# Kernel tuning notes

Hardware: AMD Instinct MI355X
Metric: run time of the kernel (lower is better)

## Reference

```python
import jax, jax.numpy as jnp
import numpy as np

B, S, NH, HID, NL = 64, 512, 16, 512, 16
W_WIN, PAD, THR, BW = 5, 2, 5.0, 0.1
D_IN = 1 + 2 * NH


def setup_inputs():
    key = jax.random.key(0)
    ks = jax.random.split(key, 16)
    time = jax.random.uniform(ks[0], (B, S)) * 1000.0
    mag = 15.0 + jax.random.normal(ks[1], (B, S))
    err = 0.01 + 0.1 * jax.random.uniform(ks[2], (B, S))
    sc = 0.05
    p = {}
    p["light_curve"] = jnp.stack([time, mag, err], axis=1)  # (B,3,S)
    p["valid_mask"] = jnp.ones((B, S), dtype=bool)
    p["frequency"] = 0.5 + 4.5 * jax.random.uniform(ks[3], (B,))
    p["W_ih0"] = sc * jax.random.normal(ks[4], (3 * HID, D_IN))
    p["b_ih0"] = jnp.zeros((3 * HID,))
    p["W_hh0"] = sc * jax.random.normal(ks[5], (3 * HID, HID))
    p["b_hh0"] = jnp.zeros((3 * HID,))
    p["W_ih1"] = sc * jax.random.normal(ks[6], (3 * HID, HID))
    p["b_ih1"] = jnp.zeros((3 * HID,))
    p["W_hh1"] = sc * jax.random.normal(ks[7], (3 * HID, HID))
    p["b_hh1"] = jnp.zeros((3 * HID,))
    p["Wl1"] = sc * jax.random.normal(ks[8], (HID, HID))
    p["bl1"] = jnp.zeros((HID,))
    p["Wl2"] = sc * jax.random.normal(ks[9], (NL, HID))
    p["bl2"] = jnp.zeros((NL,))
    return p


def _flag_outliers(phase, mag):
    # Sorted-window weighted (Epanechnikov in circular phase-delta) mean/std outlier test.
    # Caller guarantees all points valid (setup uses an all-True mask), so index_select == identity.
    perm = jnp.argsort(phase)
    ps, ms = phase[perm], mag[perm]

    def windows(x):
        xp = jnp.concatenate([x[-PAD:], x, x[:PAD]])  # circular pad
        return jnp.stack([xp[i:i + S] for i in range(W_WIN)], axis=-1)  # (S, w)

    wp, wm = windows(ps), windows(ms)
    cols = jnp.array([i for i in range(W_WIN) if i != PAD])
    dphi = wp[:, cols] - wp[:, PAD:PAD + 1]
    dphi = jnp.remainder(dphi - 0.5, 1.0) - 0.5
    wgt = 0.75 * (1.0 - dphi ** 2)
    wmm = wm[:, cols]
    wsum = wgt.sum(-1)
    loc = (wmm * wgt).sum(-1) / wsum
    scale = jnp.sqrt((((wmm - loc[:, None]) ** 2) * wgt).sum(-1) / (wsum - 1.0))
    thr = loc + THR * scale
    sigma = jnp.zeros_like(mag).at[perm].set(thr)  # inverse-permute (index_copy_)
    return mag > sigma


def _gru_layer(x, W_ih, b_ih, W_hh, b_hh):
    # torch nn.GRU cell math; x: (B,S,D) -> (B,S,H)
    xW = jnp.einsum('bsd,gd->bsg', x, W_ih) + b_ih  # (B,S,3H)

    def step(h, xt):
        hW = h @ W_hh.T + b_hh
        xr, xz, xn = jnp.split(xt, 3, axis=-1)
        hr, hz, hn = jnp.split(hW, 3, axis=-1)
        r = jax.nn.sigmoid(xr + hr)
        z = jax.nn.sigmoid(xz + hz)
        n = jnp.tanh(xn + r * hn)
        h = (1.0 - z) * n + z * h
        return h, h

    h0 = jnp.zeros((x.shape[0], W_hh.shape[1]), x.dtype)
    _, hs = jax.lax.scan(step, h0, jnp.swapaxes(xW, 0, 1))
    return jnp.swapaxes(hs, 0, 1)


def reference(light_curve, valid_mask, frequency, W_ih0, b_ih0, W_hh0, b_hh0,
              W_ih1, b_ih1, W_hh1, b_hh1, Wl1, bl1, Wl2, bl2):
    time, mag, err = light_curve[:, 0], light_curve[:, 1], light_curve[:, 2]
    period = 2.0 / frequency[:, None]  # fold_with_double_period=True (default)
    phase = jnp.remainder(time, period) / period
    outlier = jax.vmap(_flag_outliers)(phase, mag)
    is_valid = valid_mask & ~outlier

    # periodic-kernel interpolation on 50-point grid; align phase to brightness max
    grid = jnp.linspace(0.0, 1.0, 50)
    delta = grid[None, :, None] - phase[:, None, :]  # (B,50,S)
    K = jnp.exp((jnp.cos(2.0 * jnp.pi * delta) - 1.0) / BW ** 2)
    Wk = is_valid[:, None, :].astype(K.dtype) * K
    Wk = Wk / Wk.sum(-1, keepdims=True)
    smooth = (Wk * mag[:, None, :]).sum(-1)  # (B,50)
    phase = phase - grid[jnp.argmax(smooth, axis=-1)][:, None]

    # sort by phase, invalid points last; scaler=None -> loc 0, scale 1
    big = jnp.finfo(jnp.float32).max
    idx = jnp.argsort(jnp.where(is_valid, phase, big), axis=-1)
    phase = jnp.take_along_axis(phase, idx, -1)
    mag = jnp.take_along_axis(mag, idx, -1)
    is_valid = jnp.take_along_axis(is_valid, idx, -1)

    # Fourier phase embedding [cos_1..cos_H, sin_1..sin_H] + mag -> (B,S,2H+1)
    k = jnp.arange(1, NH + 1, dtype=phase.dtype)
    ang = 2.0 * jnp.pi * phase[:, :, None] * k
    emb = jnp.concatenate([jnp.cos(ang), jnp.sin(ang), mag[:, :, None]], axis=-1)

    ht = _gru_layer(emb, W_ih0, b_ih0, W_hh0, b_hh0)
    ht = _gru_layer(ht, W_ih1, b_ih1, W_hh1, b_hh1)

    m = is_valid[:, :, None].astype(ht.dtype)  # context='average'
    ctx = (ht * m).sum(1) / m.sum(1)
    h1 = jax.nn.gelu(ctx @ Wl1.T + bl1, approximate=False)
    z = h1 @ Wl2.T + bl2
    return z
```

## Files before the change

### kernel.cpp

```cpp
#include <hip/hip_runtime.h>


typedef unsigned short u16;
typedef unsigned int u32;
typedef unsigned long long u64;

__device__ __forceinline__ float b2f(u16 u) { return __uint_as_float(((u32)u) << 16); }
__device__ __forceinline__ float blo(u32 u) { return __uint_as_float(u << 16); }
__device__ __forceinline__ float bhi(u32 u) { return __uint_as_float(u & 0xffff0000u); }
__device__ __forceinline__ u16 f2b(float f) {
    u32 x = __float_as_uint(f);
    u32 r = x + 0x7fffu + ((x >> 16) & 1u);
    return (u16)(r >> 16);
}

#define SS 512
#define TWO_PI 6.28318530717958647692f
#define BIGF 3.402823466e+38f
#define PANEL_ELEMS (1536 * 512)
#define FLAGS_BYTES 32768
#define FL(g, f) (((g) * 16 + (f)) * 16)
#define F_A 0
#define F_B 2
#define F_C 4
#define G_A 6
#define G_B 8
#define G_C 10
#define F_PRE 12
#define F_CTX 14

struct P {
    const void* lc;
    const void* freq;
    const void* W[12];
    void* out;
    void* ws;
    unsigned long long ws_size;
};

__device__ __forceinline__ bool inputs_are_bf16(const void* freq) {
    const u16* q = (const u16*)freq;
    bool ok = true;
    for (int i = 0; i < 64; ++i) {
        float v = b2f(q[i]);
        ok = ok && (v >= 0.4f) && (v <= 5.5f);
    }
    return ok;
}

template<bool BF>
__device__ __forceinline__ float ldw(const void* p, size_t i) {
    if constexpr (BF) return b2f(((const u16*)p)[i]);
    else              return ((const float*)p)[i];
}
template<bool BF>
__device__ __forceinline__ const void* rowp(const void* base, int row) {
    if constexpr (BF) return (const void*)((const u16*)base + (size_t)row * 512);
    else              return (const void*)((const float*)base + (size_t)row * 512);
}

__device__ __forceinline__ void sc_store_f(float* ptr, float v) {
    __hip_atomic_store(ptr, v, __ATOMIC_RELAXED, __HIP_MEMORY_SCOPE_AGENT);
}
__device__ __forceinline__ float sc_load_f(const float* ptr) {
    return __hip_atomic_load(ptr, __ATOMIC_RELAXED, __HIP_MEMORY_SCOPE_AGENT);
}
__device__ __forceinline__ void sc_store_i(int* ptr, int v) {
    __hip_atomic_store(ptr, v, __ATOMIC_RELAXED, __HIP_MEMORY_SCOPE_AGENT);
}
__device__ __forceinline__ int sc_load_i(const int* ptr) {
    return __hip_atomic_load(ptr, __ATOMIC_RELAXED, __HIP_MEMORY_SCOPE_AGENT);
}
__device__ __forceinline__ void waitge(const int* f, int v, int* dead) {
    if (*dead) return;
    int it = 0;
    while (sc_load_i(f) < v) {
        __builtin_amdgcn_s_sleep(1);
        if (++it > 400000) { *dead = 1; break; }
    }
}

template<bool BF>
__device__ void build_panel_one(const void* W, int tid, char* panbase) {
    if constexpr (BF) {
        const uint4* Ws = (const uint4*)W;
        uint4* panel = (uint4*)panbase;
        for (int i = tid; i < 1536 * 64; i += 512) {
            int r = i >> 6, k8 = i & 63;
            panel[(size_t)k8 * 1536 + r] = Ws[i];
        }
    } else {
        const float4* Ws = (const float4*)W;
        float4* panel = (float4*)panbase;
        for (int i = tid; i < 1536 * 128; i += 512) {
            int r = i >> 7, k4 = i & 127;
            panel[(size_t)k4 * 1536 + r] = Ws[i];
        }
    }
}
template<bool BF>
__device__ void build_piece(const void* W, int half, int tid, char* panbase) {
    if constexpr (BF) {
        const uint4* Ws = (const uint4*)W;
        uint4* panel = (uint4*)panbase;
        for (int i = tid; i < 768 * 64; i += 512) {
            int r768 = i >> 6, k8 = i & 63;
            int g3 = r768 >> 8, r = r768 & 255;
            int srcrow = g3 * 512 + half * 256 + r;
            panel[(size_t)k8 * 768 + r768] = Ws[(size_t)srcrow * 64 + k8];
        }
    } else {
        const float4* Ws = (const float4*)W;
        float4* panel = (float4*)panbase;
        for (int i = tid; i < 768 * 128; i += 512) {
            int r768 = i >> 7, k4 = i & 127;
            int g3 = r768 >> 8, r = r768 & 255;
            int srcrow = g3 * 512 + half * 256 + r;
            panel[(size_t)k4 * 768 + r768] = Ws[(size_t)srcrow * 128 + k4];
        }
    }
}

template<bool BF>
__device__ __forceinline__ void tridot_panel(const void* panel, int j,
                                             const float* __restrict__ sh,
                                             float& ar, float& az, float& an) {
    if constexpr (BF) {
        const uint4* pr = (const uint4*)panel + j;
        const uint4* pz = pr + 512;
        const uint4* pn = pr + 1024;
        for (int k0 = 0; k0 < 512; k0 += 8) {
            size_t o = (size_t)(k0 >> 3) * 1536;
            float4 h0 = *(const float4*)&sh[k0];
            float4 h1 = *(const float4*)&sh[k0 + 4];
            uint4 a = pr[o], c = pz[o], d = pn[o];
            ar += blo(a.x) * h0.x + bhi(a.x) * h0.y + blo(a.y) * h0.z + bhi(a.y) * h0.w
                + blo(a.z) * h1.x + bhi(a.z) * h1.y + blo(a.w) * h1.z + bhi(a.w) * h1.w;
            az += blo(c.x) * h0.x + bhi(c.x) * h0.y + blo(c.y) * h0.z + bhi(c.y) * h0.w
                + blo(c.z) * h1.x + bhi(c.z) * h1.y + blo(c.w) * h1.z + bhi(c.w) * h1.w;
            an += blo(d.x) * h0.x + bhi(d.x) * h0.y + blo(d.y) * h0.z + bhi(d.y) * h0.w
                + blo(d.z) * h1.x + bhi(d.z) * h1.y + blo(d.w) * h1.z + bhi(d.w) * h1.w;
        }
    } else {
        const float4* pr = (const float4*)panel + j;
        const float4* pz = pr + 512;
        const float4* pn = pr + 1024;
        for (int k0 = 0; k0 < 512; k0 += 8) {
            size_t o = (size_t)(k0 >> 2) * 1536;
            float4 h0 = *(const float4*)&sh[k0];
            float4 h1 = *(const float4*)&sh[k0 + 4];
            float4 a0 = pr[o], a1 = pr[o + 1536];
            float4 c0 = pz[o], c1 = pz[o + 1536];
            float4 d0 = pn[o], d1 = pn[o + 1536];
            ar += a0.x * h0.x + a0.y * h0.y + a0.z * h0.z + a0.w * h0.w
                + a1.x * h1.x + a1.y * h1.y + a1.z * h1.z + a1.w * h1.w;
            az += c0.x * h0.x + c0.y * h0.y + c0.z * h0.z + c0.w * h0.w
                + c1.x * h1.x + c1.y * h1.y + c1.z * h1.z + c1.w * h1.w;
            an += d0.x * h0.x + d0.y * h0.y + d0.z * h0.z + d0.w * h0.w
                + d1.x * h1.x + d1.y * h1.y + d1.z * h1.z + d1.w * h1.w;
        }
    }
}

template<bool BF>
__device__ __forceinline__ void tridot2(const void* panel, int r, int kh,
                                        const float* __restrict__ ha,
                                        const float* __restrict__ hb,
                                        float& a0r, float& a0z, float& a0n,
                                        float& a1r, float& a1z, float& a1n) {
    const int kbeg = kh * 256;
    if constexpr (BF) {
        const uint4* pr = (const uint4*)panel + r;
        const uint4* pz = pr + 256;
        const uint4* pn = pr + 512;
        for (int k0 = kbeg; k0 < kbeg + 256; k0 += 8) {
            size_t o = (size_t)(k0 >> 3) * 768;
            float4 ha0 = *(const float4*)&ha[k0];
            float4 ha1 = *(const float4*)&ha[k0 + 4];
            float4 hb0 = *(const float4*)&hb[k0];
            float4 hb1 = *(const float4*)&hb[k0 + 4];
            uint4 a = pr[o], c = pz[o], d = pn[o];
            a0r += blo(a.x)*ha0.x + bhi(a.x)*ha0.y + blo(a.y)*ha0.z + bhi(a.y)*ha0.w
                 + blo(a.z)*ha1.x + bhi(a.z)*ha1.y + blo(a.w)*ha1.z + bhi(a.w)*ha1.w;
            a1r += blo(a.x)*hb0.x + bhi(a.x)*hb0.y + blo(a.y)*hb0.z + bhi(a.y)*hb0.w
                 + blo(a.z)*hb1.x + bhi(a.z)*hb1.y + blo(a.w)*hb1.z + bhi(a.w)*hb1.w;
            a0z += blo(c.x)*ha0.x + bhi(c.x)*ha0.y + blo(c.y)*ha0.z + bhi(c.y)*ha0.w
                 + blo(c.z)*ha1.x + bhi(c.z)*ha1.y + blo(c.w)*ha1.z + bhi(c.w)*ha1.w;
            a1z += blo(c.x)*hb0.x + bhi(c.x)*hb0.y + blo(c.y)*hb0.z + bhi(c.y)*hb0.w
                 + blo(c.z)*hb1.x + bhi(c.z)*hb1.y + blo(c.w)*hb1.z + bhi(c.w)*hb1.w;
            a0n += blo(d.x)*ha0.x + bhi(d.x)*ha0.y + blo(d.y)*ha0.z + bhi(d.y)*ha0.w
                 + blo(d.z)*ha1.x + bhi(d.z)*ha1.y + blo(d.w)*ha1.z + bhi(d.w)*ha1.w;
            a1n += blo(d.x)*hb0.x + bhi(d.x)*hb0.y + blo(d.y)*hb0.z + bhi(d.y)*hb0.w
                 + blo(d.z)*hb1.x + bhi(d.z)*hb1.y + blo(d.w)*hb1.z + bhi(d.w)*hb1.w;
        }
    } else {
        const float4* pr = (const float4*)panel + r;
        const float4* pz = pr + 256;
        const float4* pn = pr + 512;
        for (int k0 = kbeg; k0 < kbeg + 256; k0 += 8) {
            size_t o = (size_t)(k0 >> 2) * 768;
            float4 ha0 = *(const float4*)&ha[k0];
            float4 ha1 = *(const float4*)&ha[k0 + 4];
            float4 hb0 = *(const float4*)&hb[k0];
            float4 hb1 = *(const float4*)&hb[k0 + 4];
            float4 a0 = pr[o], a1 = pr[o + 768];
            float4 c0 = pz[o], c1 = pz[o + 768];
            float4 d0 = pn[o], d1 = pn[o + 768];
            a0r += a0.x*ha0.x + a0.y*ha0.y + a0.z*ha0.z + a0.w*ha0.w
                 + a1.x*ha1.x + a1.y*ha1.y + a1.z*ha1.z + a1.w*ha1.w;
            a1r += a0.x*hb0.x + a0.y*hb0.y + a0.z*hb0.z + a0.w*hb0.w
                 + a1.x*hb1.x + a1.y*hb1.y + a1.z*hb1.z + a1.w*hb1.w;
            a0z += c0.x*ha0.x + c0.y*ha0.y + c0.z*ha0.z + c0.w*ha0.w
                 + c1.x*ha1.x + c1.y*ha1.y + c1.z*ha1.z + c1.w*ha1.w;
            a1z += c0.x*hb0.x + c0.y*hb0.y + c0.z*hb0.z + c0.w*hb0.w
                 + c1.x*hb1.x + c1.y*hb1.y + c1.z*hb1.z + c1.w*hb1.w;
            a0n += d0.x*ha0.x + d0.y*ha0.y + d0.z*ha0.z + d0.w*ha0.w
                 + d1.x*ha1.x + d1.y*ha1.y + d1.z*ha1.z + d1.w*ha1.w;
            a1n += d0.x*hb0.x + d0.y*hb0.y + d0.z*hb0.z + d0.w*hb0.w
                 + d1.x*hb1.x + d1.y*hb1.y + d1.z*hb1.z + d1.w*hb1.w;
        }
    }
}

template<bool BF>
__device__ __forceinline__ float dot512(const void* vr, const float* __restrict__ sh) {
    float acc = 0.f;
    if constexpr (BF) {
        const u32* pr = (const u32*)vr;
        for (int k0 = 0; k0 < 512; k0 += 8) {
            float4 h0 = *(const float4*)&sh[k0];
            float4 h1 = *(const float4*)&sh[k0 + 4];
            uint4 a = *(const uint4*)(pr + (k0 >> 1));
            acc += blo(a.x) * h0.x + bhi(a.x) * h0.y + blo(a.y) * h0.z + bhi(a.y) * h0.w
                 + blo(a.z) * h1.x + bhi(a.z) * h1.y + blo(a.w) * h1.z + bhi(a.w) * h1.w;
        }
    } else {
        const float* pr = (const float*)vr;
        for (int k0 = 0; k0 < 512; k0 += 8) {
            float4 h0 = *(const float4*)&sh[k0];
            float4 h1 = *(const float4*)&sh[k0 + 4];
            float4 a0 = *(const float4*)(pr + k0), a1 = *(const float4*)(pr + k0 + 4);
            acc += a0.x * h0.x + a0.y * h0.y + a0.z * h0.z + a0.w * h0.w
                 + a1.x * h1.x + a1.y * h1.y + a1.z * h1.z + a1.w * h1.w;
        }
    }
    return acc;
}

struct PreShm {
    float ph[512], mg[512], skey[512], sig[512], vld[512];
    int   sidx[512];
    float ps2[512], ms2[512], vs2[512];
    float pn[50][8], pd[50][8], smoothv[50];
    float gshift, nv;
};

__device__ void bitonic512(float* skey, int* sidx, int tid) {
    for (int k = 2; k <= 512; k <<= 1) {
        for (int j = k >> 1; j > 0; j >>= 1) {
            int ixj = tid ^ j;
            if (ixj > tid) {
                float ka = skey[tid], kb = skey[ixj];
                int ia = sidx[tid], ib = sidx[ixj];
                bool up = ((tid & k) == 0);
                bool agtb = (ka > kb) || (ka == kb && ia > ib);
                if (agtb == up) {
                    skey[tid] = kb; skey[ixj] = ka;
                    sidx[tid] = ib; sidx[ixj] = ia;
                }
            }
            __syncthreads();
        }
    }
}

template<bool BF>
__device__ void preproc_core(const P& p, PreShm& s, int b, int tid) {
    float period = 2.0f / ldw<BF>(p.freq, b);
    float t = ldw<BF>(p.lc, (size_t)b * 3 * SS + tid);
    float m = ldw<BF>(p.lc, (size_t)b * 3 * SS + SS + tid);
    float ph0 = fmodf(t, period) / period;
    s.ph[tid] = ph0; s.mg[tid] = m;
    s.skey[tid] = ph0; s.sidx[tid] = tid;
    __syncthreads();
    bitonic512(s.skey, s.sidx, tid);
    {
        float pc = s.skey[tid];
        float wv[4], mv[4];
        float wsum = 0.f, wm = 0.f;
        const int offs[4] = {-2, -1, 1, 2};
#pragma unroll
        for (int c = 0; c < 4; ++c) {
            int jj = (tid + offs[c]) & 511;
            float d = s.skey[jj] - pc;
            float u = d - 0.5f; u = u - floorf(u);
            float dphi = u - 0.5f;
            float w = 0.75f * (1.0f - dphi * dphi);
            float mm = s.mg[s.sidx[jj]];
            wv[c] = w; mv[c] = mm;
            wsum += w; wm += w * mm;
        }
        float loc = wm / wsum;
        float s2 = 0.f;
#pragma unroll
        for (int c = 0; c < 4; ++c) { float dm = mv[c] - loc; s2 += dm * dm * wv[c]; }
        float scale = sqrtf(s2 / (wsum - 1.0f));
        s.sig[s.sidx[tid]] = loc + 5.0f * scale;
    }
    __syncthreads();
    s.vld[tid] = (s.mg[tid] > s.sig[tid]) ? 0.0f : 1.0f;
    __syncthreads();
    if (tid == 0) {
        float acc = 0.f;
        for (int i = 0; i < 512; ++i) acc += s.vld[i];
        s.nv = acc;
    }
    {
        int g = tid >> 3, pq = tid & 7;
        if (g < 50) {
            float gv = (float)g * (1.0f / 49.0f);
            float num = 0.f, den = 0.f;
            int s0 = pq * 64;
            for (int ss = s0; ss < s0 + 64; ++ss) {
                float d = gv - s.ph[ss];
                float c = cosf(TWO_PI * d);
                float K = expf((c - 1.0f) * 100.0f);
                float w = s.vld[ss] * K;
                den += w; num += w * s.mg[ss];
            }
            s.pn[g][pq] = num; s.pd[g][pq] = den;
        }
    }
    __syncthreads();
    if (tid < 50) {
        float num = 0.f, den = 0.f;
#pragma unroll
        for (int c = 0; c < 8; ++c) { num += s.pn[tid][c]; den += s.pd[tid][c]; }
        s.smoothv[tid] = num / den;
    }
    __syncthreads();
    if (tid == 0) {
        float best = s.smoothv[0]; int bi = 0;
        for (int g = 1; g < 50; ++g) if (s.smoothv[g] > best) { best = s.smoothv[g]; bi = g; }
        s.gshift = (float)bi * (1.0f / 49.0f);
    }
    __syncthreads();
    float p2 = s.ph[tid] - s.gshift;
    s.ph[tid] = p2;
    s.skey[tid] = (s.vld[tid] > 0.f) ? p2 : BIGF;
    s.sidx[tid] = tid;
    __syncthreads();
    bitonic512(s.skey, s.sidx, tid);
    {
        int o = s.sidx[tid];
        s.ps2[tid] = s.ph[o]; s.ms2[tid] = s.mg[o]; s.vs2[tid] = s.vld[o];
    }
    __syncthreads();
}

struct ShmA {
    PreShm pre;
    float psb[2][512], msb[2][512];
    float h0L[1024];
    float eL[2][34];
    float part[6][256];
    float xp[3][256];
};
struct ShmB { float h0loc[1024]; float part[6][256]; };
struct ShmC {
    float h1L[1024]; float vs2L[2][512]; float nvL[2];
    float ctxL[512], gL[512]; float part[6][256];
};
struct ShmOldA { PreShm pre; float h0[512], h1[512], eL[34]; };
struct ShmU {
    union { ShmA a; ShmB b; ShmC c; ShmOldA o; } u;
    int dead;
};

template<bool BF, bool PAN>
__device__ void run_all(const P& p, ShmU& S) {
    PreShm& pre = S.u.o.pre;
    float* h0 = S.u.o.h0;
    float* h1 = S.u.o.h1;
    float* eL = S.u.o.eL;
    int b = blockIdx.x, tid = threadIdx.x;
    char* panbase = (char*)p.ws + FLAGS_BYTES;
    const size_t PMAT = (size_t)PANEL_ELEMS * (BF ? 2 : 4);

    if constexpr (PAN) {
        build_panel_one<BF>(p.W[2], tid, panbase);
        build_panel_one<BF>(p.W[4], tid, panbase + PMAT);
        build_panel_one<BF>(p.W[6], tid, panbase + 2 * PMAT);
        __threadfence();
    }
    preproc_core<BF>(p, pre, b, tid);

    int j = tid;
    float wr0[33], wz0[33], wn0[33];
#pragma unroll
    for (int d = 0; d < 33; ++d) {
        wr0[d] = ldw<BF>(p.W[0], (size_t)j * 33 + d);
        wz0[d] = ldw<BF>(p.W[0], ((size_t)j + 512) * 33 + d);
        wn0[d] = ldw<BF>(p.W[0], ((size_t)j + 1024) * 33 + d);
    }
    float bi0r = ldw<BF>(p.W[1], j), bi0z = ldw<BF>(p.W[1], j + 512), bi0n = ldw<BF>(p.W[1], j + 1024);
    float bh0r = ldw<BF>(p.W[3], j), bh0z = ldw<BF>(p.W[3], j + 512), bh0n = ldw<BF>(p.W[3], j + 1024);
    float bi1r = ldw<BF>(p.W[5], j), bi1z = ldw<BF>(p.W[5], j + 512), bi1n = ldw<BF>(p.W[5], j + 1024);
    float bh1r = ldw<BF>(p.W[7], j), bh1z = ldw<BF>(p.W[7], j + 512), bh1n = ldw<BF>(p.W[7], j + 1024);

    const void* pan0  = (const void*)panbase;
    const void* pan1x = (const void*)(panbase + PMAT);
    const void* pan1h = (const void*)(panbase + 2 * PMAT);
    const void *w0r = rowp<BF>(p.W[2], j), *w0z = rowp<BF>(p.W[2], j + 512), *w0n = rowp<BF>(p.W[2], j + 1024);
    const void *x1r = rowp<BF>(p.W[4], j), *x1z = rowp<BF>(p.W[4], j + 512), *x1n = rowp<BF>(p.W[4], j + 1024);
    const void *w1r = rowp<BF>(p.W[6], j), *w1z = rowp<BF>(p.W[6], j + 512), *w1n = rowp<BF>(p.W[6], j + 1024);

    h0[j] = 0.f; h1[j] = 0.f;
    float cacc = 0.f;
    __syncthreads();

    for (int tt = 0; tt < 512; ++tt) {
        if (j < 16) {
            float ang = TWO_PI * pre.ps2[tt] * (float)(j + 1);
            float sv, cv; sincosf(ang, &sv, &cv);
            eL[j] = cv; eL[16 + j] = sv;
        }
        if (j == 32) eL[32] = pre.ms2[tt];
        __syncthreads();
        float xr = bi0r, xz = bi0z, xn = bi0n;
#pragma unroll
        for (int d = 0; d < 33; ++d) {
            float e = eL[d];
            xr += wr0[d] * e; xz += wz0[d] * e; xn += wn0[d] * e;
        }
        float ar = bh0r, az = bh0z, an = bh0n;
        if constexpr (PAN) tridot_panel<BF>(pan0, j, h0, ar, az, an);
        else {
            for (int k = 0; k < 512; ++k) {
                float h = h0[k];
                ar += ldw<BF>(w0r, k) * h; az += ldw<BF>(w0z, k) * h; an += ldw<BF>(w0n, k) * h;
            }
        }
        float h0prev = h0[j];
        float r0 = 1.0f / (1.0f + expf(-(xr + ar)));
        float z0 = 1.0f / (1.0f + expf(-(xz + az)));
        float n0 = tanhf(xn + r0 * an);
        float nh0 = (1.0f - z0) * n0 + z0 * h0prev;
        __syncthreads();
        h0[j] = nh0;
        __syncthreads();
        float yr = bi1r, yz = bi1z, yn = bi1n;
        float cr = bh1r, cz = bh1z, cn = bh1n;
        if constexpr (PAN) {
            tridot_panel<BF>(pan1x, j, h0, yr, yz, yn);
            tridot_panel<BF>(pan1h, j, h1, cr, cz, cn);
        } else {
            for (int k = 0; k < 512; ++k) {
                float h = h0[k], g = h1[k];
                yr += ldw<BF>(x1r, k) * h; yz += ldw<BF>(x1z, k) * h; yn += ldw<BF>(x1n, k) * h;
                cr += ldw<BF>(w1r, k) * g; cz += ldw<BF>(w1z, k) * g; cn += ldw<BF>(w1n, k) * g;
            }
        }
        float h1prev = h1[j];
        float r1 = 1.0f / (1.0f + expf(-(yr + cr)));
        float z1 = 1.0f / (1.0f + expf(-(yz + cz)));
        float n1 = tanhf(yn + r1 * cn);
        float nh1 = (1.0f - z1) * n1 + z1 * h1prev;
        cacc += pre.vs2[tt] * nh1;
        __syncthreads();
        h1[j] = nh1;
    }
    __syncthreads();

    h0[j] = cacc / pre.nv;
    __syncthreads();
    float a1 = ldw<BF>(p.W[9], j) + dot512<BF>(rowp<BF>(p.W[8], j), h0);
    float g = 0.5f * a1 * (1.0f + erff(a1 * 0.70710678118654752440f));
    __syncthreads();
    h1[j] = g;
    __syncthreads();
    if (j < 16) {
        float a2 = ldw<BF>(p.W[11], j) + dot512<BF>(rowp<BF>(p.W[10], j), h1);
        if constexpr (BF) ((u16*)p.out)[(size_t)b * 16 + j] = f2b(a2);
        else              ((float*)p.out)[(size_t)b * 16 + j] = a2;
    }
}

__global__ __launch_bounds__(512) void fused_kernel_old(P p) {
    __shared__ ShmU S;
    bool bf = inputs_are_bf16(p.freq);
    u64 PMAT = bf ? 1572864ull : 3145728ull;
    bool pan = (p.ws && p.ws_size >= (u64)FLAGS_BYTES + 3 * PMAT);
    if (bf) { if (pan) run_all<true, true>(p, S);  else run_all<true, false>(p, S); }
    else    { if (pan) run_all<false, true>(p, S); else run_all<false, false>(p, S); }
}


template<bool BF>
__device__ void runA(const P& p, ShmU& S, int g, int hf, int tid, char* pan,
                     float* h0r, float* pp, int* flags) {
    int* dead = &S.dead;
    build_piece<BF>(p.W[2], hf, tid, pan);
    __threadfence();
    int myb = 2 * g + hf, ob = 2 * g + (1 - hf);
    preproc_core<BF>(p, S.u.a.pre, myb, tid);
    sc_store_f(&pp[(size_t)myb * 2048 + tid], S.u.a.pre.ps2[tid]);
    sc_store_f(&pp[(size_t)myb * 2048 + 512 + tid], S.u.a.pre.ms2[tid]);
    sc_store_f(&pp[(size_t)myb * 2048 + 1024 + tid], S.u.a.pre.vs2[tid]);
    if (tid == 0) sc_store_f(&pp[(size_t)myb * 2048 + 1536], S.u.a.pre.nv);
    asm volatile("s_waitcnt vmcnt(0)" ::: "memory");
    __syncthreads();
    if (tid == 0) sc_store_i(&flags[FL(g, F_PRE + hf)], 1);
    S.u.a.psb[hf][tid] = S.u.a.pre.ps2[tid];
    S.u.a.msb[hf][tid] = S.u.a.pre.ms2[tid];
    if (tid == 0) waitge(&flags[FL(g, F_PRE + (1 - hf))], 1, dead);
    __syncthreads();
    S.u.a.psb[1 - hf][tid] = sc_load_f(&pp[(size_t)ob * 2048 + tid]);
    S.u.a.msb[1 - hf][tid] = sc_load_f(&pp[(size_t)ob * 2048 + 512 + tid]);

    const int r = tid & 255, kh = tid >> 8;
    const int j = hf * 256 + r;
    const float bi0r = ldw<BF>(p.W[1], j), bi0z = ldw<BF>(p.W[1], j + 512), bi0n = ldw<BF>(p.W[1], j + 1024);
    const float bh0r = ldw<BF>(p.W[3], j), bh0z = ldw<BF>(p.W[3], j + 512), bh0n = ldw<BF>(p.W[3], j + 1024);

    float* h0L = S.u.a.h0L;
    h0L[tid] = 0.f; h0L[tid + 512] = 0.f;
    __syncthreads();

    for (int t = 0; t < 512; ++t) {
        if (tid < 16) {
            float ang = TWO_PI * S.u.a.psb[0][t] * (float)(tid + 1);
            float sv, cv; sincosf(ang, &sv, &cv);
            S.u.a.eL[0][tid] = cv; S.u.a.eL[0][16 + tid] = sv;
        } else if (tid < 32) {
            int k = tid - 16;
            float ang = TWO_PI * S.u.a.psb[1][t] * (float)(k + 1);
            float sv, cv; sincosf(ang, &sv, &cv);
            S.u.a.eL[1][k] = cv; S.u.a.eL[1][16 + k] = sv;
        }
        if (tid == 32) S.u.a.eL[0][32] = S.u.a.msb[0][t];
        if (tid == 33) S.u.a.eL[1][32] = S.u.a.msb[1][t];
        if (t > 0 && tid == 0) waitge(&flags[FL(g, F_A + (1 - hf))], t, dead);
        __syncthreads();

        float sib = 0.f;
        if (t > 0)
            sib = sc_load_f(&h0r[(size_t)g * 2048 + ((t - 1) & 1) * 1024 + (1 - hf) * 512 + kh * 256 + r]);
        float xr = bi0r, xz = bi0z, xn = bi0n;
#pragma unroll
        for (int d = 0; d < 33; ++d) {
            float e = S.u.a.eL[kh][d];
            xr += ldw<BF>(p.W[0], (size_t)j * 33 + d) * e;
            xz += ldw<BF>(p.W[0], ((size_t)j + 512) * 33 + d) * e;
            xn += ldw<BF>(p.W[0], ((size_t)j + 1024) * 33 + d) * e;
        }
        if (t > 0) h0L[kh * 512 + (1 - hf) * 256 + r] = sib;
        __syncthreads();
        if (t > 0 && tid == 0) sc_store_i(&flags[FL(g, G_A + hf)], t);

        float p0r = 0.f, p0z = 0.f, p0n = 0.f, p1r = 0.f, p1z = 0.f, p1n = 0.f;
        tridot2<BF>(pan, r, kh, &h0L[0], &h0L[512], p0r, p0z, p0n, p1r, p1z, p1n);
        if (kh == 1) {
            S.u.a.part[0][r] = p0r; S.u.a.part[1][r] = p0z; S.u.a.part[2][r] = p0n;
            S.u.a.part[3][r] = p1r; S.u.a.part[4][r] = p1z; S.u.a.part[5][r] = p1n;
            S.u.a.xp[0][r] = xr; S.u.a.xp[1][r] = xz; S.u.a.xp[2][r] = xn;
        }
        __syncthreads();
        float nh00 = 0.f, nh01 = 0.f;
        if (kh == 0) {
            float ar0 = bh0r + p0r + S.u.a.part[0][r];
            float az0 = bh0z + p0z + S.u.a.part[1][r];
            float an0 = bh0n + p0n + S.u.a.part[2][r];
            float ar1 = bh0r + p1r + S.u.a.part[3][r];
            float az1 = bh0z + p1z + S.u.a.part[4][r];
            float an1 = bh0n + p1n + S.u.a.part[5][r];
            float x1r = S.u.a.xp[0][r], x1z = S.u.a.xp[1][r], x1n = S.u.a.xp[2][r];
            float h0p0 = h0L[j], h0p1 = h0L[512 + j];
            float r0 = 1.f / (1.f + expf(-(xr + ar0)));
            float z0 = 1.f / (1.f + expf(-(xz + az0)));
            float n0 = tanhf(xn + r0 * an0);
            nh00 = (1.f - z0) * n0 + z0 * h0p0;
            float r1 = 1.f / (1.f + expf(-(x1r + ar1)));
            float z1 = 1.f / (1.f + expf(-(x1z + az1)));
            float n1 = tanhf(x1n + r1 * an1);
            nh01 = (1.f - z1) * n1 + z1 * h0p1;
            h0L[j] = nh00; h0L[512 + j] = nh01;
        }
        if (t >= 2) {
            if (tid == 0) waitge(&flags[FL(g, G_A + (1 - hf))], t - 1, dead);
            if (tid == 1) waitge(&flags[FL(g, G_B + 0)], t - 1, dead);
            if (tid == 2) waitge(&flags[FL(g, G_B + 1)], t - 1, dead);
        }
        __syncthreads();
        if (kh == 0) {
            float* dst = &h0r[(size_t)g * 2048 + (t & 1) * 1024 + hf * 512];
            sc_store_f(&dst[r], nh00);
            sc_store_f(&dst[256 + r], nh01);
        }
        asm volatile("s_waitcnt vmcnt(0)" ::: "memory");
        __syncthreads();
        if (tid == 0) sc_store_i(&flags[FL(g, F_A + hf)], t + 1);
    }
}

template<bool BF>
__device__ void runB(const P& p, ShmU& S, int g, int hf, int tid, char* pan,
                     float* h0r, float* yrng, int* flags) {
    int* dead = &S.dead;
    build_piece<BF>(p.W[4], hf, tid, pan);
    __threadfence();
    __syncthreads();
    const int r = tid & 255, kh = tid >> 8;
    const int j = hf * 256 + r;
    const float bi1r = ldw<BF>(p.W[5], j), bi1z = ldw<BF>(p.W[5], j + 512), bi1n = ldw<BF>(p.W[5], j + 1024);
    float* h0loc = S.u.b.h0loc;

    for (int t = 0; t < 512; ++t) {
        if (tid == 0) waitge(&flags[FL(g, F_A + 0)], t + 1, dead);
        if (tid == 1) waitge(&flags[FL(g, F_A + 1)], t + 1, dead);
        __syncthreads();
        const float* src = &h0r[(size_t)g * 2048 + (t & 1) * 1024];
        h0loc[kh * 512 + r]       = sc_load_f(&src[0 * 512 + kh * 256 + r]);
        h0loc[kh * 512 + 256 + r] = sc_load_f(&src[1 * 512 + kh * 256 + r]);
        __syncthreads();
        if (tid == 0) sc_store_i(&flags[FL(g, G_B + hf)], t + 1);
        float p0r = 0.f, p0z = 0.f, p0n = 0.f, p1r = 0.f, p1z = 0.f, p1n = 0.f;
        tridot2<BF>(pan, r, kh, &h0loc[0], &h0loc[512], p0r, p0z, p0n, p1r, p1z, p1n);
        if (kh == 1) {
            S.u.b.part[0][r] = p0r; S.u.b.part[1][r] = p0z; S.u.b.part[2][r] = p0n;
            S.u.b.part[3][r] = p1r; S.u.b.part[4][r] = p1z; S.u.b.part[5][r] = p1n;
        }
        if (tid == 0 && t >= 2) waitge(&flags[FL(g, G_C + hf)], t - 1, dead);
        __syncthreads();
        if (kh == 0) {
            float y0r = bi1r + p0r + S.u.b.part[0][r];
            float y0z = bi1z + p0z + S.u.b.part[1][r];
            float y0n = bi1n + p0n + S.u.b.part[2][r];
            float y1r = bi1r + p1r + S.u.b.part[3][r];
            float y1z = bi1z + p1z + S.u.b.part[4][r];
            float y1n = bi1n + p1n + S.u.b.part[5][r];
            float* slot = &yrng[(size_t)g * 6144 + (t & 1) * 3072 + hf * 1536];
            sc_store_f(&slot[r], y0r);         sc_store_f(&slot[256 + r], y1r);
            sc_store_f(&slot[512 + r], y0z);   sc_store_f(&slot[768 + r], y1z);
            sc_store_f(&slot[1024 + r], y0n);  sc_store_f(&slot[1280 + r], y1n);
        }
        asm volatile("s_waitcnt vmcnt(0)" ::: "memory");
        __syncthreads();
        if (tid == 0) sc_store_i(&flags[FL(g, F_B + hf)], t + 1);
    }
}

template<bool BF>
__device__ void runC(const P& p, ShmU& S, int g, int hf, int tid, char* pan,
                     float* yrng, float* h1r, float* pp, float* ctxb, int* flags) {
    int* dead = &S.dead;
    build_piece<BF>(p.W[6], hf, tid, pan);
    __threadfence();
    if (tid == 0) waitge(&flags[FL(g, F_PRE + 0)], 1, dead);
    if (tid == 1) waitge(&flags[FL(g, F_PRE + 1)], 1, dead);
    __syncthreads();
    S.u.c.vs2L[0][tid] = sc_load_f(&pp[(size_t)(2 * g) * 2048 + 1024 + tid]);
    S.u.c.vs2L[1][tid] = sc_load_f(&pp[(size_t)(2 * g + 1) * 2048 + 1024 + tid]);
    if (tid == 0) {
        S.u.c.nvL[0] = sc_load_f(&pp[(size_t)(2 * g) * 2048 + 1536]);
        S.u.c.nvL[1] = sc_load_f(&pp[(size_t)(2 * g + 1) * 2048 + 1536]);
    }
    float* h1L = S.u.c.h1L;
    h1L[tid] = 0.f; h1L[tid + 512] = 0.f;
    __syncthreads();

    const int r = tid & 255, kh = tid >> 8;
    const int j = hf * 256 + r;
    const float bh1r = ldw<BF>(p.W[7], j), bh1z = ldw<BF>(p.W[7], j + 512), bh1n = ldw<BF>(p.W[7], j + 1024);
    float cacc0 = 0.f, cacc1 = 0.f;

    for (int t = 0; t < 512; ++t) {
        if (t > 0 && tid == 1) waitge(&flags[FL(g, F_C + (1 - hf))], t, dead);
        __syncthreads();
        if (t > 0) {
            h1L[kh * 512 + (1 - hf) * 256 + r] =
                sc_load_f(&h1r[(size_t)g * 2048 + ((t - 1) & 1) * 1024 + (1 - hf) * 512 + kh * 256 + r]);
        }
        __syncthreads();

        float p0r = 0.f, p0z = 0.f, p0n = 0.f, p1r = 0.f, p1z = 0.f, p1n = 0.f;
        tridot2<BF>(pan, r, kh, &h1L[0], &h1L[512], p0r, p0z, p0n, p1r, p1z, p1n);
        if (kh == 1) {
            S.u.c.part[0][r] = p0r; S.u.c.part[1][r] = p0z; S.u.c.part[2][r] = p0n;
            S.u.c.part[3][r] = p1r; S.u.c.part[4][r] = p1z; S.u.c.part[5][r] = p1n;
        }
        if (tid == 0) waitge(&flags[FL(g, F_B + hf)], t + 1, dead);
        __syncthreads();

        float nh10 = 0.f, nh11 = 0.f;
        if (kh == 0) {
            const float* slot = &yrng[(size_t)g * 6144 + (t & 1) * 3072 + hf * 1536];
            float y0r = sc_load_f(&slot[r]);         float y1r = sc_load_f(&slot[256 + r]);
            float y0z = sc_load_f(&slot[512 + r]);   float y1z = sc_load_f(&slot[768 + r]);
            float y0n = sc_load_f(&slot[1024 + r]);  float y1n = sc_load_f(&slot[1280 + r]);
            float cr0 = bh1r + p0r + S.u.c.part[0][r];
            float cz0 = bh1z + p0z + S.u.c.part[1][r];
            float cn0 = bh1n + p0n + S.u.c.part[2][r];
            float cr1 = bh1r + p1r + S.u.c.part[3][r];
            float cz1 = bh1z + p1z + S.u.c.part[4][r];
            float cn1 = bh1n + p1n + S.u.c.part[5][r];
            float h1p0 = h1L[j], h1p1 = h1L[512 + j];
            float r0 = 1.f / (1.f + expf(-(y0r + cr0)));
            float z0 = 1.f / (1.f + expf(-(y0z + cz0)));
            float n0 = tanhf(y0n + r0 * cn0);
            nh10 = (1.f - z0) * n0 + z0 * h1p0;
            float r1 = 1.f / (1.f + expf(-(y1r + cr1)));
            float z1 = 1.f / (1.f + expf(-(y1z + cz1)));
            float n1 = tanhf(y1n + r1 * cn1);
            nh11 = (1.f - z1) * n1 + z1 * h1p1;
            cacc0 += S.u.c.vs2L[0][t] * nh10;
            cacc1 += S.u.c.vs2L[1][t] * nh11;
        }
        __syncthreads();
        if (tid == 0) sc_store_i(&flags[FL(g, G_C + hf)], t + 1);
        if (kh == 0) { h1L[j] = nh10; h1L[512 + j] = nh11; }
        if (t >= 2 && tid == 2) waitge(&flags[FL(g, G_C + (1 - hf))], t, dead);
        __syncthreads();
        if (kh == 0) {
            float* dst = &h1r[(size_t)g * 2048 + (t & 1) * 1024 + hf * 512];
            sc_store_f(&dst[r], nh10);
            sc_store_f(&dst[256 + r], nh11);
        }
        asm volatile("s_waitcnt vmcnt(0)" ::: "memory");
        __syncthreads();
        if (tid == 0) sc_store_i(&flags[FL(g, F_C + hf)], t + 1);
    }

    if (kh == 0) {
        sc_store_f(&ctxb[(size_t)g * 1024 + hf * 512 + r], cacc0);
        sc_store_f(&ctxb[(size_t)g * 1024 + hf * 512 + 256 + r], cacc1);
    }
    asm volatile("s_waitcnt vmcnt(0)" ::: "memory");
    __syncthreads();
    if (tid == 0) {
        sc_store_i(&flags[FL(g, F_CTX + hf)], 1);
        waitge(&flags[FL(g, F_CTX + (1 - hf))], 1, dead);
    }
    __syncthreads();
    float nv = S.u.c.nvL[hf];
    S.u.c.ctxL[tid] = sc_load_f(&ctxb[(size_t)g * 1024 + (tid >> 8) * 512 + hf * 256 + (tid & 255)]) / nv;
    __syncthreads();
    float a1 = ldw<BF>(p.W[9], tid) + dot512<BF>(rowp<BF>(p.W[8], tid), S.u.c.ctxL);
    float gg = 0.5f * a1 * (1.0f + erff(a1 * 0.70710678118654752440f));
    __syncthreads();
    S.u.c.gL[tid] = gg;
    __syncthreads();
    if (tid < 16) {
        float a2 = ldw<BF>(p.W[11], tid) + dot512<BF>(rowp<BF>(p.W[10], tid), S.u.c.gL);
        int hb = 2 * g + hf;
        if constexpr (BF) ((u16*)p.out)[(size_t)hb * 16 + tid] = f2b(a2);
        else              ((float*)p.out)[(size_t)hb * 16 + tid] = a2;
    }
}

template<bool BF>
__device__ void run_pipe(const P& p, ShmU& S) {
    const int bid = blockIdx.x;
    const int piece = bid & 7;
    if (piece >= 6) return;
    const int g = bid >> 3;
    const int role = piece >> 1, hf = piece & 1;
    const int tid = threadIdx.x;
    if (tid == 0) S.dead = 0;
    __syncthreads();

    char* wsb = (char*)p.ws;
    int* flags = (int*)wsb;
    const size_t PIECE = BF ? 786432 : 1572864;
    char* pans = wsb + FLAGS_BYTES;
    char* mypan = pans + (size_t)piece * PIECE;
    float* h0r  = (float*)(pans + 6 * PIECE);
    float* yrng = h0r + (size_t)32 * 2048;
    float* h1r  = yrng + (size_t)32 * 6144;
    float* pp   = h1r + (size_t)32 * 2048;
    float* ctxb = pp + (size_t)64 * 2048;

    if (role == 0)      runA<BF>(p, S, g, hf, tid, mypan, h0r, pp, flags);
    else if (role == 1) runB<BF>(p, S, g, hf, tid, mypan, h0r, yrng, flags);
    else                runC<BF>(p, S, g, hf, tid, mypan, yrng, h1r, pp, ctxb, flags);
}

__global__ __launch_bounds__(512) void fused_kernel_pipe(P p) {
    __shared__ ShmU S;
    if (inputs_are_bf16(p.freq)) run_pipe<true>(p, S);
    else                         run_pipe<false>(p, S);
}

extern "C" void kernel_launch(void* const* d_in, const int* in_sizes, int n_in,
                              void* d_out, int out_size, void* d_ws, size_t ws_size,
                              hipStream_t stream) {
    P p;
    p.lc = d_in[0];
    p.freq = d_in[2];
    for (int i = 0; i < 12; ++i) p.W[i] = d_in[3 + i];
    p.out = d_out;
    p.ws = d_ws;
    p.ws_size = (unsigned long long)ws_size;

    const size_t need_pipe = 11436032ull;
    if (d_ws && ws_size >= need_pipe) {
        hipMemsetAsync(d_ws, 0, FLAGS_BYTES, stream);
        fused_kernel_pipe<<<256, 512, 0, stream>>>(p);
    } else {
        fused_kernel_old<<<64, 512, 0, stream>>>(p);
    }
    (void)in_sizes; (void)n_in; (void)out_size;
}
```

Baseline: 12.41 ms.

## Overlap own-half recurrent dot product with sibling hidden-state exchange wait

Splits each thread's recurrent matvec over k into the half owned by this block (already local) and the half produced by the sibling block. The own half is computed before waiting for and loading the sibling's hidden state, so the inter-block flag spin and global load overlap with useful work in both GRU layers. It reorders barriers around the exchange, and the k ranges are reassigned so each thread covers 128 own and 128 sibling columns. This risks subtle synchronisation hazards if the h buffers are overwritten while still being read.

```diff
diff --git a/kernel.cpp b/kernel.cpp
--- a/kernel.cpp
+++ b/kernel.cpp
@@ -163,17 +163,16 @@
 }
 
 template<bool BF>
-__device__ __forceinline__ void tridot2(const void* panel, int r, int kh,
-                                        const float* __restrict__ ha,
-                                        const float* __restrict__ hb,
-                                        float& a0r, float& a0z, float& a0n,
-                                        float& a1r, float& a1z, float& a1n) {
-    const int kbeg = kh * 256;
+__device__ __forceinline__ void tridot2r(const void* panel, int r, int kb,
+                                         const float* __restrict__ ha,
+                                         const float* __restrict__ hb,
+                                         float& a0r, float& a0z, float& a0n,
+                                         float& a1r, float& a1z, float& a1n) {
     if constexpr (BF) {
         const uint4* pr = (const uint4*)panel + r;
         const uint4* pz = pr + 256;
         const uint4* pn = pr + 512;
-        for (int k0 = kbeg; k0 < kbeg + 256; k0 += 8) {
+        for (int k0 = kb; k0 < kb + 128; k0 += 8) {
             size_t o = (size_t)(k0 >> 3) * 768;
             float4 ha0 = *(const float4*)&ha[k0];
             float4 ha1 = *(const float4*)&ha[k0 + 4];
@@ -197,7 +196,7 @@
         const float4* pr = (const float4*)panel + r;
         const float4* pz = pr + 256;
         const float4* pn = pr + 512;
-        for (int k0 = kbeg; k0 < kbeg + 256; k0 += 8) {
+        for (int k0 = kb; k0 < kb + 128; k0 += 8) {
             size_t o = (size_t)(k0 >> 2) * 768;
             float4 ha0 = *(const float4*)&ha[k0];
             float4 ha1 = *(const float4*)&ha[k0 + 4];
@@ -223,6 +222,16 @@
 }
 
 template<bool BF>
+__device__ __forceinline__ void tridot2(const void* panel, int r, int kh,
+                                        const float* __restrict__ ha,
+                                        const float* __restrict__ hb,
+                                        float& a0r, float& a0z, float& a0n,
+                                        float& a1r, float& a1z, float& a1n) {
+    tridot2r<BF>(panel, r, kh * 256,       ha, hb, a0r, a0z, a0n, a1r, a1z, a1n);
+    tridot2r<BF>(panel, r, kh * 256 + 128, ha, hb, a0r, a0z, a0n, a1r, a1z, a1n);
+}
+
+template<bool BF>
 __device__ __forceinline__ float dot512(const void* vr, const float* __restrict__ sh) {
     float acc = 0.f;
     if constexpr (BF) {
@@ -523,6 +532,9 @@
     const float bi0r = ldw<BF>(p.W[1], j), bi0z = ldw<BF>(p.W[1], j + 512), bi0n = ldw<BF>(p.W[1], j + 1024);
     const float bh0r = ldw<BF>(p.W[3], j), bh0z = ldw<BF>(p.W[3], j + 512), bh0n = ldw<BF>(p.W[3], j + 1024);
 
+    const int kOwn = hf * 256 + kh * 128;
+    const int kSib = (1 - hf) * 256 + kh * 128;
+
     float* h0L = S.u.a.h0L;
     h0L[tid] = 0.f; h0L[tid + 512] = 0.f;
     __syncthreads();
@@ -540,12 +552,9 @@
         }
         if (tid == 32) S.u.a.eL[0][32] = S.u.a.msb[0][t];
         if (tid == 33) S.u.a.eL[1][32] = S.u.a.msb[1][t];
+        __syncthreads();
+
         if (t > 0 && tid == 0) waitge(&flags[FL(g, F_A + (1 - hf))], t, dead);
-        __syncthreads();
-
-        float sib = 0.f;
-        if (t > 0)
-            sib = sc_load_f(&h0r[(size_t)g * 2048 + ((t - 1) & 1) * 1024 + (1 - hf) * 512 + kh * 256 + r]);
         float xr = bi0r, xz = bi0z, xn = bi0n;
 #pragma unroll
         for (int d = 0; d < 33; ++d) {
@@ -554,18 +563,25 @@
             xz += ldw<BF>(p.W[0], ((size_t)j + 512) * 33 + d) * e;
             xn += ldw<BF>(p.W[0], ((size_t)j + 1024) * 33 + d) * e;
         }
-        if (t > 0) h0L[kh * 512 + (1 - hf) * 256 + r] = sib;
+        float p0r = 0.f, p0z = 0.f, p0n = 0.f, p1r = 0.f, p1z = 0.f, p1n = 0.f;
+        tridot2r<BF>(pan, r, kOwn, &h0L[0], &h0L[512], p0r, p0z, p0n, p1r, p1z, p1n);
+        __syncthreads();
+
+        if (t > 0) {
+            h0L[kh * 512 + (1 - hf) * 256 + r] =
+                sc_load_f(&h0r[(size_t)g * 2048 + ((t - 1) & 1) * 1024 + (1 - hf) * 512 + kh * 256 + r]);
+        }
         __syncthreads();
         if (t > 0 && tid == 0) sc_store_i(&flags[FL(g, G_A + hf)], t);
 
-        float p0r = 0.f, p0z = 0.f, p0n = 0.f, p1r = 0.f, p1z = 0.f, p1n = 0.f;
-        tridot2<BF>(pan, r, kh, &h0L[0], &h0L[512], p0r, p0z, p0n, p1r, p1z, p1n);
+        tridot2r<BF>(pan, r, kSib, &h0L[0], &h0L[512], p0r, p0z, p0n, p1r, p1z, p1n);
         if (kh == 1) {
             S.u.a.part[0][r] = p0r; S.u.a.part[1][r] = p0z; S.u.a.part[2][r] = p0n;
             S.u.a.part[3][r] = p1r; S.u.a.part[4][r] = p1z; S.u.a.part[5][r] = p1n;
             S.u.a.xp[0][r] = xr; S.u.a.xp[1][r] = xz; S.u.a.xp[2][r] = xn;
         }
         __syncthreads();
+
         float nh00 = 0.f, nh01 = 0.f;
         if (kh == 0) {
             float ar0 = bh0r + p0r + S.u.a.part[0][r];
@@ -672,19 +688,23 @@
     const int r = tid & 255, kh = tid >> 8;
     const int j = hf * 256 + r;
     const float bh1r = ldw<BF>(p.W[7], j), bh1z = ldw<BF>(p.W[7], j + 512), bh1n = ldw<BF>(p.W[7], j + 1024);
+    const int kOwn = hf * 256 + kh * 128;
+    const int kSib = (1 - hf) * 256 + kh * 128;
     float cacc0 = 0.f, cacc1 = 0.f;
 
     for (int t = 0; t < 512; ++t) {
         if (t > 0 && tid == 1) waitge(&flags[FL(g, F_C + (1 - hf))], t, dead);
-        __syncthreads();
+        float p0r = 0.f, p0z = 0.f, p0n = 0.f, p1r = 0.f, p1z = 0.f, p1n = 0.f;
+        tridot2r<BF>(pan, r, kOwn, &h1L[0], &h1L[512], p0r, p0z, p0n, p1r, p1z, p1n);
+        __syncthreads();
+
         if (t > 0) {
             h1L[kh * 512 + (1 - hf) * 256 + r] =
                 sc_load_f(&h1r[(size_t)g * 2048 + ((t - 1) & 1) * 1024 + (1 - hf) * 512 + kh * 256 + r]);
         }
         __syncthreads();
 
-        float p0r = 0.f, p0z = 0.f, p0n = 0.f, p1r = 0.f, p1z = 0.f, p1n = 0.f;
-        tridot2<BF>(pan, r, kh, &h1L[0], &h1L[512], p0r, p0z, p0n, p1r, p1z, p1n);
+        tridot2r<BF>(pan, r, kSib, &h1L[0], &h1L[512], p0r, p0z, p0n, p1r, p1z, p1n);
         if (kh == 1) {
             S.u.c.part[0][r] = p0r; S.u.c.part[1][r] = p0z; S.u.c.part[2][r] = p0n;
             S.u.c.part[3][r] = p1r; S.u.c.part[4][r] = p1z; S.u.c.part[5][r] = p1n;
```

Result: no change. 12.48 ms (+0.6%).
